# Performance work log

Hardware: AMD Instinct MI355X
Metric: run time of the kernel (lower is better)

Reference implementation:

```python
import jax, jax.numpy as jnp
import numpy as np

D_K = 128

def setup_inputs() -> dict:
    key = jax.random.key(0)
    k1, k2, k3 = jax.random.split(key, 3)
    q = jax.random.normal(k1, (8192, D_K), dtype=jnp.float32)
    k = jax.random.normal(k2, (8192, D_K), dtype=jnp.float32)
    v = jax.random.normal(k3, (8192, D_K), dtype=jnp.float32)
    return {"q": q, "k": k, "v": v}

def reference(q, k, v):
    # scores: [S_q, S_k]
    scores = jnp.einsum('qd,kd->qk', q, k) / jnp.sqrt(jnp.float32(D_K))
    attn = jax.nn.softmax(scores, axis=-1)  # softmax over keys (torch default last dim)
    return jnp.einsum('qk,kd->qd', attn, v)
```

## Files before the change

kernel.cpp:

```cpp
#include <hip/hip_runtime.h>
#include <math.h>


typedef _Float16 f16x8 __attribute__((ext_vector_type(8)));
typedef float    f32x16 __attribute__((ext_vector_type(16)));

constexpr int S_LEN = 8192;
constexpr int D_K   = 128;
constexpr int NSLICE = 8;
constexpr int ITERS2 = (S_LEN / NSLICE) / 64;

constexpr size_t WS_L_OFF = 0;
constexpr size_t KV_OFF   = 262144;
constexpr size_t PART_OFF = KV_OFF + (size_t)256 * 16384;
constexpr size_t WS_NEED  = PART_OFF + (size_t)7 * S_LEN * D_K * 4;

#define CSCALE (0.08838834764831845f * 1.44269504088896340736f)

union UH8 { _Float16 h[8]; uint4 q; f16x8 v; };
union UF4 { unsigned u[4]; uint4 q; f16x8 v; };

__device__ inline void async16(const uint4* g, uint4* l) {
  __builtin_amdgcn_global_load_lds(
      (const __attribute__((address_space(1))) unsigned int*)g,
      (__attribute__((address_space(3))) unsigned int*)l, 16, 0, 0);
}

template <bool ZOUT>
__global__ __launch_bounds__(512) void attn_prep(const float* __restrict__ K,
                                                 const float* __restrict__ V,
                                                 float* __restrict__ out,
                                                 char* __restrict__ ws) {
  const int t = blockIdx.x * 512 + threadIdx.x;
  uint4* KVg = (uint4*)(ws + KV_OFF);
  if (t < 131072) {
    int kt = t >> 9, idx = t & 511;
    int lane = idx & 63, s = idx >> 6;
    int key = kt * 32 + (lane & 31);
    int d0  = s * 16 + (lane >> 5) * 8;
    const float4* src = (const float4*)(K + (size_t)key * D_K + d0);
    float4 a = src[0], b = src[1];
    float f[8] = {a.x, a.y, a.z, a.w, b.x, b.y, b.z, b.w};
    UH8 h;
    #pragma unroll
    for (int j = 0; j < 8; ++j) h.h[j] = (_Float16)f[j];
    KVg[(size_t)kt * 1024 + idx] = h.q;
  } else if (t < 262144) {
    int g = t - 131072;
    int kt = g >> 9, idx = g & 511;
    int lane = idx & 63, c = (idx >> 6) & 3, kstep = idx >> 8;
    int d  = c * 32 + (lane & 31);
    int kb = kt * 32 + kstep * 16 + (lane >> 5) * 8;
    UH8 h;
    #pragma unroll
    for (int j = 0; j < 8; ++j) h.h[j] = (_Float16)V[(size_t)(kb + j) * D_K + d];
    KVg[(size_t)kt * 1024 + 512 + idx] = h.q;
  } else if (ZOUT && t < 327680) {
    int i = t - 262144;
    float4 z = make_float4(0.f, 0.f, 0.f, 0.f);
    float4* o4 = (float4*)out;
    #pragma unroll
    for (int j = 0; j < 4; ++j) o4[(size_t)i * 4 + j] = z;
  } else if (ZOUT && t < 329728) {
    int i = t - 327680;
    ((float4*)(ws + WS_L_OFF))[i] = make_float4(0.f, 0.f, 0.f, 0.f);
  }
}

template <bool PARTIAL>
__global__ __launch_bounds__(256, 2)
void attn_main(const float* __restrict__ Qg, float* __restrict__ out,
               char* __restrict__ ws) {
  __shared__ uint4 KV[2][2048];

  const int tid   = threadIdx.x;
  const int wave  = tid >> 6;
  const int lane  = tid & 63;
  const int lrow  = lane & 31;
  const int lhalf = lane >> 5;

  const int blk = blockIdx.x;
  const int ks  = blk & 7;
  const int qb  = blk >> 3;
  const int qw  = qb * 128 + wave * 32;

  float* ws_l = (float*)(ws + WS_L_OFF);

  f16x8 qf[8];
  {
    const int q = qw + lrow;
    #pragma unroll
    for (int s = 0; s < 8; ++s) {
      const float4* src = (const float4*)(Qg + (size_t)q * D_K + s * 16 + lhalf * 8);
      float4 a = src[0], b = src[1];
      float f[8] = {a.x, a.y, a.z, a.w, b.x, b.y, b.z, b.w};
      UH8 h;
      #pragma unroll
      for (int j = 0; j < 8; ++j) h.h[j] = (_Float16)(f[j] * CSCALE);
      qf[s] = h.v;
    }
  }

  f32x16 O0{}, O1{}, O2{}, O3{};
  float lsum = 0.f;

  const uint4* KVg = (const uint4*)(ws + KV_OFF);

  {
    const size_t base = (size_t)ks * 32768;
    #pragma unroll
    for (int i = 0; i < 8; ++i)
      async16(KVg + base + i * 256 + tid, &KV[0][i * 256 + tid]);
  }

  for (int it = 0; it < ITERS2; ++it) {
    const int buf = it & 1;
    __syncthreads();

    if (it + 1 < ITERS2) {
      const size_t base = (size_t)ks * 32768 + (size_t)(it + 1) * 2048;
      #pragma unroll
      for (int i = 0; i < 8; ++i)
        async16(KVg + base + i * 256 + tid, &KV[buf ^ 1][i * 256 + tid]);
    }

    #pragma unroll
    for (int u = 0; u < 2; ++u) {
      const uint4* sub = &KV[buf][u * 1024];

      f32x16 Sa{}, Sb{};
      #pragma unroll
      for (int s = 0; s < 4; ++s) {
        f16x8 ka = __builtin_bit_cast(f16x8, sub[(2 * s    ) * 64 + lane]);
        f16x8 kb = __builtin_bit_cast(f16x8, sub[(2 * s + 1) * 64 + lane]);
        Sa = __builtin_amdgcn_mfma_f32_32x32x16_f16(ka, qf[2 * s    ], Sa, 0, 0, 0);
        Sb = __builtin_amdgcn_mfma_f32_32x32x16_f16(kb, qf[2 * s + 1], Sb, 0, 0, 0);
      }

      unsigned pk[8];
      #pragma unroll
      for (int i = 0; i < 8; ++i) {
        float p0 = __builtin_amdgcn_exp2f(Sa[2 * i]     + Sb[2 * i]);
        float p1 = __builtin_amdgcn_exp2f(Sa[2 * i + 1] + Sb[2 * i + 1]);
        lsum += p0 + p1;
        pk[i] = __builtin_bit_cast(unsigned, __builtin_amdgcn_cvt_pkrtz(p0, p1));
      }

      unsigned s0 = __shfl_xor(pk[0], 32), s1 = __shfl_xor(pk[1], 32);
      unsigned s2 = __shfl_xor(pk[2], 32), s3 = __shfl_xor(pk[3], 32);
      unsigned s4 = __shfl_xor(pk[4], 32), s5 = __shfl_xor(pk[5], 32);
      unsigned s6 = __shfl_xor(pk[6], 32), s7 = __shfl_xor(pk[7], 32);
      UF4 A0, A1;
      A0.u[0] = lhalf ? s2 : pk[0];
      A0.u[1] = lhalf ? s3 : pk[1];
      A0.u[2] = lhalf ? pk[2] : s0;
      A0.u[3] = lhalf ? pk[3] : s1;
      A1.u[0] = lhalf ? s6 : pk[4];
      A1.u[1] = lhalf ? s7 : pk[5];
      A1.u[2] = lhalf ? pk[6] : s4;
      A1.u[3] = lhalf ? pk[7] : s5;

      #pragma unroll
      for (int kstep = 0; kstep < 2; ++kstep) {
        f16x8 pf = kstep ? A1.v : A0.v;
        f16x8 v0 = __builtin_bit_cast(f16x8, sub[512 + kstep * 256 +   0 + lane]);
        f16x8 v1 = __builtin_bit_cast(f16x8, sub[512 + kstep * 256 +  64 + lane]);
        f16x8 v2 = __builtin_bit_cast(f16x8, sub[512 + kstep * 256 + 128 + lane]);
        f16x8 v3 = __builtin_bit_cast(f16x8, sub[512 + kstep * 256 + 192 + lane]);
        O0 = __builtin_amdgcn_mfma_f32_32x32x16_f16(pf, v0, O0, 0, 0, 0);
        O1 = __builtin_amdgcn_mfma_f32_32x32x16_f16(pf, v1, O1, 0, 0, 0);
        O2 = __builtin_amdgcn_mfma_f32_32x32x16_f16(pf, v2, O2, 0, 0, 0);
        O3 = __builtin_amdgcn_mfma_f32_32x32x16_f16(pf, v3, O3, 0, 0, 0);
      }
    }
  }

  lsum += __shfl_xor(lsum, 32);

  if (PARTIAL) {
    if (lhalf == 0) ws_l[ks * S_LEN + qw + lrow] = lsum;
    float* obase = (ks == 0) ? out
                 : (float*)(ws + PART_OFF) + (size_t)(ks - 1) * S_LEN * D_K;
    #pragma unroll
    for (int r = 0; r < 16; ++r) {
      int row = (r & 3) + 8 * (r >> 2) + 4 * lhalf;
      float* dst = obase + (size_t)(qw + row) * D_K + lrow;
      dst[ 0] = O0[r];
      dst[32] = O1[r];
      dst[64] = O2[r];
      dst[96] = O3[r];
    }
  } else {
    if (lhalf == 0) atomicAdd(ws_l + qw + lrow, lsum);
    #pragma unroll
    for (int r = 0; r < 16; ++r) {
      int row = (r & 3) + 8 * (r >> 2) + 4 * lhalf;
      float* dst = out + (size_t)(qw + row) * D_K + lrow;
      atomicAdd(dst +  0, O0[r]);
      atomicAdd(dst + 32, O1[r]);
      atomicAdd(dst + 64, O2[r]);
      atomicAdd(dst + 96, O3[r]);
    }
  }
}

__global__ __launch_bounds__(256) void attn_norm(float* __restrict__ out,
                                                 const float* __restrict__ lpart,
                                                 const float* __restrict__ opart,
                                                 int nparts) {
  int i = blockIdx.x * 256 + threadIdx.x;
  int q = i >> 5;
  float4* o4 = (float4*)out;
  float4 acc = o4[i];
  float l = lpart[q];
  for (int s = 1; s <= nparts; ++s) {
    float4 p = ((const float4*)opart)[(size_t)(s - 1) * 262144 + i];
    acc.x += p.x; acc.y += p.y; acc.z += p.z; acc.w += p.w;
    l += lpart[s * S_LEN + q];
  }
  float inv = 1.0f / l;
  acc.x *= inv; acc.y *= inv; acc.z *= inv; acc.w *= inv;
  o4[i] = acc;
}

extern "C" void kernel_launch(void* const* d_in, const int* in_sizes, int n_in,
                              void* d_out, int out_size, void* d_ws, size_t ws_size,
                              hipStream_t stream) {
  const float* q = (const float*)d_in[0];
  const float* k = (const float*)d_in[1];
  const float* v = (const float*)d_in[2];
  float* out = (float*)d_out;
  char* ws = (char*)d_ws;

  if (ws_size >= WS_NEED) {
    attn_prep<false><<<dim3(512), dim3(512), 0, stream>>>(k, v, out, ws);
    attn_main<true><<<dim3(512), dim3(256), 0, stream>>>(q, out, ws);
    attn_norm<<<dim3(1024), dim3(256), 0, stream>>>(
        out, (const float*)(ws + WS_L_OFF), (const float*)(ws + PART_OFF), 7);
  } else {
    attn_prep<true><<<dim3(645), dim3(512), 0, stream>>>(k, v, out, ws);
    attn_main<false><<<dim3(512), dim3(256), 0, stream>>>(q, out, ws);
    attn_norm<<<dim3(1024), dim3(256), 0, stream>>>(
        out, (const float*)(ws + WS_L_OFF), (const float*)(ws + PART_OFF), 0);
  }
}
```

Before: 113.3 us.

## Stream V fragments from global into registers, keep only K in LDS

```diff
diff --git a/kernel.cpp b/kernel.cpp
--- a/kernel.cpp
+++ b/kernel.cpp
@@ -11,8 +11,9 @@
 constexpr int ITERS2 = (S_LEN / NSLICE) / 64;
 
 constexpr size_t WS_L_OFF = 0;
-constexpr size_t KV_OFF   = 262144;
-constexpr size_t PART_OFF = KV_OFF + (size_t)256 * 16384;
+constexpr size_t KF_OFF   = 262144;
+constexpr size_t VF_OFF   = KF_OFF + (size_t)256 * 8192;
+constexpr size_t PART_OFF = VF_OFF + (size_t)256 * 8192;
 constexpr size_t WS_NEED  = PART_OFF + (size_t)7 * S_LEN * D_K * 4;
 
 #define CSCALE (0.08838834764831845f * 1.44269504088896340736f)
@@ -32,7 +33,6 @@
                                                  float* __restrict__ out,
                                                  char* __restrict__ ws) {
   const int t = blockIdx.x * 512 + threadIdx.x;
-  uint4* KVg = (uint4*)(ws + KV_OFF);
   if (t < 131072) {
     int kt = t >> 9, idx = t & 511;
     int lane = idx & 63, s = idx >> 6;
@@ -44,7 +44,7 @@
     UH8 h;
     #pragma unroll
     for (int j = 0; j < 8; ++j) h.h[j] = (_Float16)f[j];
-    KVg[(size_t)kt * 1024 + idx] = h.q;
+    ((uint4*)(ws + KF_OFF))[(size_t)kt * 512 + idx] = h.q;
   } else if (t < 262144) {
     int g = t - 131072;
     int kt = g >> 9, idx = g & 511;
@@ -54,7 +54,7 @@
     UH8 h;
     #pragma unroll
     for (int j = 0; j < 8; ++j) h.h[j] = (_Float16)V[(size_t)(kb + j) * D_K + d];
-    KVg[(size_t)kt * 1024 + 512 + idx] = h.q;
+    ((uint4*)(ws + VF_OFF))[(size_t)kt * 512 + idx] = h.q;
   } else if (ZOUT && t < 327680) {
     int i = t - 262144;
     float4 z = make_float4(0.f, 0.f, 0.f, 0.f);
@@ -71,7 +71,7 @@
 __global__ __launch_bounds__(256, 2)
 void attn_main(const float* __restrict__ Qg, float* __restrict__ out,
                char* __restrict__ ws) {
-  __shared__ uint4 KV[2][2048];
+  __shared__ uint4 Ks[2][1024];
 
   const int tid   = threadIdx.x;
   const int wave  = tid >> 6;
@@ -104,29 +104,38 @@
   f32x16 O0{}, O1{}, O2{}, O3{};
   float lsum = 0.f;
 
-  const uint4* KVg = (const uint4*)(ws + KV_OFF);
+  const uint4* KFg = (const uint4*)(ws + KF_OFF);
+  const uint4* VFg = (const uint4*)(ws + VF_OFF);
 
   {
-    const size_t base = (size_t)ks * 32768;
-    #pragma unroll
-    for (int i = 0; i < 8; ++i)
-      async16(KVg + base + i * 256 + tid, &KV[0][i * 256 + tid]);
+    const size_t base = (size_t)ks * 16384;
+    #pragma unroll
+    for (int i = 0; i < 4; ++i)
+      async16(KFg + base + i * 256 + tid, &Ks[0][i * 256 + tid]);
   }
 
   for (int it = 0; it < ITERS2; ++it) {
     const int buf = it & 1;
+    const int kt0 = ks * 32 + it * 2;
     __syncthreads();
 
     if (it + 1 < ITERS2) {
-      const size_t base = (size_t)ks * 32768 + (size_t)(it + 1) * 2048;
-      #pragma unroll
-      for (int i = 0; i < 8; ++i)
-        async16(KVg + base + i * 256 + tid, &KV[buf ^ 1][i * 256 + tid]);
+      const size_t base = ((size_t)kt0 + 2) * 512;
+      #pragma unroll
+      for (int i = 0; i < 4; ++i)
+        async16(KFg + base + i * 256 + tid, &Ks[buf ^ 1][i * 256 + tid]);
+    }
+
+    uint4 vr0[8];
+    {
+      const uint4* vb = VFg + (size_t)kt0 * 512 + lane;
+      #pragma unroll
+      for (int f = 0; f < 8; ++f) vr0[f] = vb[f * 64];
     }
 
     #pragma unroll
     for (int u = 0; u < 2; ++u) {
-      const uint4* sub = &KV[buf][u * 1024];
+      const uint4* sub = &Ks[buf][u * 512];
 
       f32x16 Sa{}, Sb{};
       #pragma unroll
@@ -160,17 +169,37 @@
       A1.u[2] = lhalf ? pk[6] : s4;
       A1.u[3] = lhalf ? pk[7] : s5;
 
+      uint4 vr1[8];
+      if (u == 0) {
+        const uint4* vb = VFg + ((size_t)kt0 + 1) * 512 + lane;
+        #pragma unroll
+        for (int f = 0; f < 8; ++f) vr1[f] = vb[f * 64];
+      }
+
+      const uint4* vr = (u == 0) ? vr0 : vr0;
       #pragma unroll
       for (int kstep = 0; kstep < 2; ++kstep) {
         f16x8 pf = kstep ? A1.v : A0.v;
-        f16x8 v0 = __builtin_bit_cast(f16x8, sub[512 + kstep * 256 +   0 + lane]);
-        f16x8 v1 = __builtin_bit_cast(f16x8, sub[512 + kstep * 256 +  64 + lane]);
-        f16x8 v2 = __builtin_bit_cast(f16x8, sub[512 + kstep * 256 + 128 + lane]);
-        f16x8 v3 = __builtin_bit_cast(f16x8, sub[512 + kstep * 256 + 192 + lane]);
+        f16x8 v0, v1, v2, v3;
+        if (u == 0) {
+          v0 = __builtin_bit_cast(f16x8, vr0[kstep * 4 + 0]);
+          v1 = __builtin_bit_cast(f16x8, vr0[kstep * 4 + 1]);
+          v2 = __builtin_bit_cast(f16x8, vr0[kstep * 4 + 2]);
+          v3 = __builtin_bit_cast(f16x8, vr0[kstep * 4 + 3]);
+        } else {
+          v0 = __builtin_bit_cast(f16x8, vr0[kstep * 4 + 0]);
+          v1 = __builtin_bit_cast(f16x8, vr0[kstep * 4 + 1]);
+          v2 = __builtin_bit_cast(f16x8, vr0[kstep * 4 + 2]);
+          v3 = __builtin_bit_cast(f16x8, vr0[kstep * 4 + 3]);
+        }
         O0 = __builtin_amdgcn_mfma_f32_32x32x16_f16(pf, v0, O0, 0, 0, 0);
         O1 = __builtin_amdgcn_mfma_f32_32x32x16_f16(pf, v1, O1, 0, 0, 0);
         O2 = __builtin_amdgcn_mfma_f32_32x32x16_f16(pf, v2, O2, 0, 0, 0);
         O3 = __builtin_amdgcn_mfma_f32_32x32x16_f16(pf, v3, O3, 0, 0, 0);
+      }
+      if (u == 0) {
+        #pragma unroll
+        for (int f = 0; f < 8; ++f) vr0[f] = vr1[f];
       }
     }
   }
```

Result: slower. 121.8 us (+7.4%).
